# Kernel optimization log

Hardware: AMD Instinct MI355X
Metric: run time of the kernel (lower is better)

## Reference

```python
import jax, jax.numpy as jnp
import numpy as np

# dims: batch B, tokens T, model_dim D, expert hidden H, experts E, top-k K
B, T, D, H, E, K = 4, 2048, 2048, 2048, 8, 2
CAP_FACTOR = 1.0
S = B * T
C = int(np.ceil(K * S / E * CAP_FACTOR))  # per-expert capacity = 2048


def setup_inputs() -> dict:
    key = jax.random.key(0)
    k0, k1, k2, k3 = jax.random.split(key, 4)
    x = jax.random.normal(k0, (B, T, D), dtype=jnp.float32)
    wg = jax.random.normal(k1, (D, E), dtype=jnp.float32) * (D ** -0.5)
    w1 = jax.random.normal(k2, (E, D, H), dtype=jnp.float32) * (D ** -0.5)
    b1 = jnp.zeros((E, H), dtype=jnp.float32)
    w2 = jax.random.normal(k3, (E, H, D), dtype=jnp.float32) * (H ** -0.5)
    b2 = jnp.zeros((E, D), dtype=jnp.float32)
    return {"x": x, "wg": wg, "w1": w1, "b1": b1, "w2": w2, "b2": b2}


def _moe(x, wg, w1, b1, w2, b2):
    xt = x.reshape(S, D)
    # --- top-k gating (deepspeed-style, gates normalized over selected k) ---
    gates = jax.nn.softmax(xt @ wg, axis=-1)            # [S,E]
    vals, idx = jax.lax.top_k(gates, K)                 # [S,K]
    vals = vals / jnp.sum(vals, axis=-1, keepdims=True)
    # --- capacity-aware slot assignment (slot j offset by counts of slots < j) ---
    m = jax.nn.one_hot(idx, E, dtype=jnp.int32).transpose(1, 0, 2)  # [K,S,E]
    within = jnp.cumsum(m, axis=1) - m                  # 0-based rank within expert per slot
    counts = jnp.sum(m, axis=1)                         # [K,E]
    offs = jnp.cumsum(counts, axis=0) - counts          # [K,E] offsets from earlier slots
    loc = jnp.sum((within + offs[:, None, :]) * m, axis=2)  # [K,S]
    eid = idx.T                                         # [K,S]
    valid = loc < C
    loc_c = jnp.minimum(loc, C - 1)
    # --- dispatch: scatter raw tokens into [E,C,D] expert buffers ---
    contrib = jnp.where(valid[..., None], xt[None, :, :], 0.0)   # [K,S,D]
    disp = jnp.zeros((E, C, D), x.dtype).at[eid, loc_c].add(contrib)
    # --- grouped expert FFN: relu(x @ W1 + b1) @ W2 + b2 ---
    h = jax.nn.relu(jnp.einsum('ecd,edh->ech', disp, w1) + b1[:, None, :])
    ye = jnp.einsum('ech,ehd->ecd', h, w2) + b2[:, None, :]
    # --- combine: gather expert outputs, weight by normalized gates ---
    gathered = ye[eid, loc_c]                           # [K,S,D]
    w = (vals.T * valid).astype(x.dtype)                # [K,S]
    out = jnp.einsum('ks,ksd->sd', w, gathered)
    return out.reshape(B, T, D)


def reference(x, wg, w1, b1, w2, b2):
    y = _moe(x, wg, w1, b1, w2, b2)                     # [B,T,D]
    return jax.nn.log_softmax(jnp.sum(y, axis=2), axis=1)  # [B,T]
```

## Files before the change

### kernel.cpp

```cpp
#include <hip/hip_runtime.h>
#include <math.h>

#define S_TOK 8192
#define DDIM 2048
#define HDIM 2048
#define NE 8
#define CAP 2048
#define NBATCH 4
#define TT 2048

typedef _Float16 f16;
typedef _Float16 f16x4 __attribute__((ext_vector_type(4)));
typedef _Float16 f16x8 __attribute__((ext_vector_type(8)));
typedef float f32x4 __attribute__((ext_vector_type(4)));

typedef __attribute__((address_space(1))) const void* gas_ptr;
typedef __attribute__((address_space(3))) void* las_ptr;

#define W1T_BLOCKS 8192
#define W2S_BLOCKS 4096
#define GATE_BASE (W1T_BLOCKS + W2S_BLOCKS + 1)
#define K1_GRID (GATE_BASE + S_TOK / 4)

__global__ __launch_bounds__(256) void prep_kernel(const float* __restrict__ w1,
                                                   const float* __restrict__ w2,
                                                   const float* __restrict__ b2,
                                                   const float* __restrict__ x,
                                                   const float* __restrict__ wg,
                                                   int* __restrict__ eid,
                                                   float* __restrict__ wts,
                                                   int* __restrict__ slot_token,
                                                   float* __restrict__ zacc,
                                                   f16* __restrict__ W1T,
                                                   float* __restrict__ w2s,
                                                   float* __restrict__ b2s) {
  __shared__ float tile[64 * 65];
  int bid = blockIdx.x, tid = threadIdx.x;
  if (bid >= GATE_BASE) {
    int g = bid - GATE_BASE;
    if (g < 64) {
      int i = g * 256 + tid;
      slot_token[i] = 0;
      zacc[i] = 0.f;
    }
    int wid = tid >> 6;
    int lane = tid & 63;
    int s = g * 4 + wid;
    const float* xr = x + (size_t)s * DDIM;
    double acc[8];
#pragma unroll
    for (int e = 0; e < 8; ++e) acc[e] = 0.0;
    for (int d0 = 0; d0 < DDIM; d0 += 64) {
      float xs = xr[d0 + lane];
      const float4* wp = (const float4*)(wg + (size_t)(d0 + lane) * 8);
      float4 g0 = wp[0];
      float4 g1 = wp[1];
      double xd = (double)xs;
      acc[0] += xd * (double)g0.x; acc[1] += xd * (double)g0.y;
      acc[2] += xd * (double)g0.z; acc[3] += xd * (double)g0.w;
      acc[4] += xd * (double)g1.x; acc[5] += xd * (double)g1.y;
      acc[6] += xd * (double)g1.z; acc[7] += xd * (double)g1.w;
    }
#pragma unroll
    for (int e = 0; e < 8; ++e) {
      double v = acc[e];
      for (int off = 32; off > 0; off >>= 1) v += __shfl_down(v, off, 64);
      acc[e] = v;
    }
    if (lane == 0) {
      int e0 = 0; double l0 = acc[0];
      for (int e = 1; e < 8; ++e) if (acc[e] > l0) { l0 = acc[e]; e0 = e; }
      int e1 = -1; double l1 = -1e300;
      for (int e = 0; e < 8; ++e) if (e != e0 && acc[e] > l1) { l1 = acc[e]; e1 = e; }
      double pe = exp(l1 - l0);
      double inv = 1.0 / (1.0 + pe);
      eid[2 * s] = e0; eid[2 * s + 1] = e1;
      wts[2 * s] = (float)inv; wts[2 * s + 1] = (float)(pe * inv);
    }
    return;
  }
  if (bid < W1T_BLOCKS) {
    int e = bid >> 10, rem = bid & 1023;
    int d0 = (rem >> 5) << 6;
    int h0 = (rem & 31) << 6;
    const float* w1e = w1 + (size_t)e * DDIM * HDIM;
#pragma unroll
    for (int i = 0; i < 4; ++i) {
      int linear = i * 256 + tid;
      int r = linear >> 4, c4 = linear & 15;
      float4 v = *(const float4*)(w1e + (size_t)(d0 + r) * HDIM + h0 + c4 * 4);
      float* t = &tile[r * 65 + c4 * 4];
      t[0] = v.x; t[1] = v.y; t[2] = v.z; t[3] = v.w;
    }
    __syncthreads();
    f16* W1Te = W1T + (size_t)e * HDIM * DDIM;
#pragma unroll
    for (int i = 0; i < 2; ++i) {
      int linear = i * 256 + tid;
      int hr = linear >> 3, l8 = linear & 7;
      f16x8 o;
#pragma unroll
      for (int j = 0; j < 8; ++j) o[j] = (f16)tile[(l8 * 8 + j) * 65 + hr];
      *(f16x8*)(W1Te + (size_t)(h0 + hr) * DDIM + d0 + l8 * 8) = o;
    }
    return;
  }
  if (bid < W1T_BLOCKS + W2S_BLOCKS) {
    int wid = tid >> 6, lane = tid & 63;
    int row = (bid - W1T_BLOCKS) * 4 + wid;
    const float4* w24 = (const float4*)w2;
    float acc = 0.f;
    for (int j = 0; j < 8; ++j) {
      float4 v = w24[(size_t)row * 512 + j * 64 + lane];
      acc += v.x + v.y + v.z + v.w;
    }
    for (int off = 32; off > 0; off >>= 1) acc += __shfl_down(acc, off, 64);
    if (lane == 0) w2s[row] = acc;
    return;
  }
  {
    int e = tid >> 5, l32 = tid & 31;
    float acc = 0.f;
    for (int j = 0; j < 64; ++j) acc += b2[e * 2048 + j * 32 + l32];
    for (int off = 16; off > 0; off >>= 1) acc += __shfl_down(acc, off, 32);
    if (l32 == 0) b2s[e] = acc;
  }
}

__global__ __launch_bounds__(256) void scan_kernel(const int* __restrict__ eid,
                                                   int* __restrict__ locb,
                                                   int* __restrict__ slot_token) {
  __shared__ int seg[4][2][8];
  __shared__ int base[4][2][8];
  int tid = threadIdx.x, wid = tid >> 6, lane = tid & 63;
  unsigned long long lower = (lane == 0) ? 0ull : ((~0ull) >> (64 - lane));
  const int2* eid2 = (const int2*)eid;
  int c0 = 0, c1 = 0;
  for (int r = 0; r < 32; ++r) {
    int2 ee = eid2[wid * 2048 + r * 64 + lane];
#pragma unroll
    for (int e = 0; e < 8; ++e) {
      unsigned long long b0 = __ballot(ee.x == e);
      unsigned long long b1 = __ballot(ee.y == e);
      if (lane == e) { c0 += __popcll(b0); c1 += __popcll(b1); }
    }
  }
  if (lane < 8) { seg[wid][0][lane] = c0; seg[wid][1][lane] = c1; }
  __syncthreads();
  if (lane < 8) {
    int e = lane;
    int tot0 = seg[0][0][e] + seg[1][0][e] + seg[2][0][e] + seg[3][0][e];
    int b0 = 0, b1 = tot0;
    for (int w = 0; w < wid; ++w) { b0 += seg[w][0][e]; b1 += seg[w][1][e]; }
    base[wid][0][e] = b0; base[wid][1][e] = b1;
  }
  for (int r = 0; r < 32; ++r) {
    int2 ee = eid2[wid * 2048 + r * 64 + lane];
    int rank0 = 0, rank1 = 0, add0 = 0, add1 = 0;
#pragma unroll
    for (int e = 0; e < 8; ++e) {
      unsigned long long b0 = __ballot(ee.x == e);
      unsigned long long b1 = __ballot(ee.y == e);
      if (ee.x == e) rank0 = __popcll(b0 & lower);
      if (ee.y == e) rank1 = __popcll(b1 & lower);
      if (lane == e) { add0 = __popcll(b0); add1 = __popcll(b1); }
    }
    int loc0 = base[wid][0][ee.x] + rank0;
    int loc1 = base[wid][1][ee.y] + rank1;
    int s = wid * 2048 + r * 64 + lane;
    int2 lo; lo.x = loc0; lo.y = loc1;
    *(int2*)&locb[2 * s] = lo;
    if (loc0 < CAP) slot_token[ee.x * CAP + loc0] = s;
    if (loc1 < CAP) slot_token[ee.y * CAP + loc1] = s;
    if (lane < 8) {
      atomicAdd(&base[wid][0][lane], add0);
      atomicAdd(&base[wid][1][lane], add1);
    }
  }
}

__global__ __launch_bounds__(256) void abuild_kernel(const float* __restrict__ x,
                                                     const int* __restrict__ slot_token,
                                                     f16* __restrict__ A16) {
  int wid = threadIdx.x >> 6, lane = threadIdx.x & 63;
  int slot = blockIdx.x * 4 + wid;
  int s = slot_token[slot];
  const float4* x4 = (const float4*)x + (size_t)s * 512 + lane;
  f16x4* outp = (f16x4*)(A16 + (size_t)slot * DDIM) + lane;
#pragma unroll
  for (int i = 0; i < 8; ++i) {
    float4 xv = x4[i * 64];
    f16x4 h;
    h[0] = (f16)xv.x; h[1] = (f16)xv.y; h[2] = (f16)xv.z; h[3] = (f16)xv.w;
    outp[i * 64] = h;
  }
}


template <int MB, int NB>
__device__ __forceinline__ void quad_mfma(f32x4 (&acc)[8][4], const f16x8 (&av)[4][2],
                                          const f16x8 (&bv)[2][2]) {
#pragma unroll
  for (int mf = 0; mf < 4; ++mf)
#pragma unroll
    for (int nf = 0; nf < 2; ++nf) {
      f32x4 c = acc[MB + mf][NB + nf];
      c = __builtin_amdgcn_mfma_f32_16x16x32_f16(av[mf][0], bv[nf][0], c, 0, 0, 0);
      c = __builtin_amdgcn_mfma_f32_16x16x32_f16(av[mf][1], bv[nf][1], c, 0, 0, 0);
      acc[MB + mf][NB + nf] = c;
    }
}

__device__ __forceinline__ void lda4(f16x8 (&av)[4][2], const f16* p0, const f16* p1, int mh) {
#pragma unroll
  for (int mf = 0; mf < 4; ++mf) {
    av[mf][0] = *(const f16x8*)(p0 + (mh * 4 + mf) * 1024);
    av[mf][1] = *(const f16x8*)(p1 + (mh * 4 + mf) * 1024);
  }
}
__device__ __forceinline__ void ldb2(f16x8 (&bv)[2][2], const f16* p0, const f16* p1, int nh) {
#pragma unroll
  for (int nf = 0; nf < 2; ++nf) {
    bv[nf][0] = *(const f16x8*)(p0 + (nh * 2 + nf) * 1024);
    bv[nf][1] = *(const f16x8*)(p1 + (nh * 2 + nf) * 1024);
  }
}

__device__ __forceinline__ void stage_half(const f16* tile_rows, f16* lds_region,
                                           int T, int h, int wl8, int wu8, int cs) {
#pragma unroll
  for (int i = 0; i < 2; ++i) {
    const f16* g = tile_rows + (size_t)(h * 128 + i * 64 + wl8) * DDIM + T * 64 + cs * 8;
    f16* d = lds_region + (h * 128 + i * 64 + wu8) * 64;
    __builtin_amdgcn_global_load_lds((gas_ptr)g, (las_ptr)d, 16, 0, 0);
  }
}

__device__ __forceinline__ void bar() {
  asm volatile("" ::: "memory");
  __builtin_amdgcn_s_barrier();
  asm volatile("" ::: "memory");
}
__device__ __forceinline__ void mfma_open() {
  bar();
  asm volatile("s_waitcnt lgkmcnt(0)" ::: "memory");
  __builtin_amdgcn_sched_barrier(0);
  __builtin_amdgcn_s_setprio(1);
}
__device__ __forceinline__ void mfma_close() {
  __builtin_amdgcn_s_setprio(0);
  bar();
}
__device__ __forceinline__ void mfma_close_w4() {
  __builtin_amdgcn_s_setprio(0);
  asm volatile("s_waitcnt vmcnt(4)" ::: "memory");
  bar();
}
__device__ __forceinline__ void mfma_close_w0() {
  __builtin_amdgcn_s_setprio(0);
  asm volatile("s_waitcnt vmcnt(0)" ::: "memory");
  bar();
}

__global__ __launch_bounds__(512, 2) void gemm_kernel(const f16* __restrict__ A16,
                                                      const f16* __restrict__ W1T,
                                                      const float* __restrict__ b1,
                                                      const float* __restrict__ w2s,
                                                      float* __restrict__ zacc) {
  __shared__ __align__(16) f16 lds[4 * 256 * 64];
  const int tid = threadIdx.x;
  const int wid = tid >> 6, lane = tid & 63;
  const int wm = wid >> 2, wn = wid & 3;
  const int quad = lane >> 4, l15 = lane & 15;
  const int l3 = lane >> 3, c7 = lane & 7;
  const int cs = c7 ^ l3;
  const int wl8 = wid * 8 + l3, wu8 = wid * 8;

  int bid = blockIdx.x;
  int e = bid & 7;
  int idx = bid >> 3;
  int cT = idx >> 3, hT = idx & 7;
  int c0 = cT * 256, h0 = hT * 256;

  const f16* Abase = A16 + ((size_t)e * CAP + c0) * DDIM;
  const f16* Bbase = W1T + ((size_t)e * HDIM + h0) * DDIM;

  f16* bufA0 = &lds[0];
  f16* bufB0 = &lds[16384];
  f16* bufA1 = &lds[2 * 16384];
  f16* bufB1 = &lds[3 * 16384];

  const int so0 = (quad ^ c7) * 8;
  const int so1 = ((quad + 4) ^ c7) * 8;
  const f16* a0k0 = bufA0 + (wm * 128 + l15) * 64 + so0;
  const f16* a0k1 = bufA0 + (wm * 128 + l15) * 64 + so1;
  const f16* a1k0 = a0k0 + 2 * 16384;
  const f16* a1k1 = a0k1 + 2 * 16384;
  const f16* b0k0 = bufB0 + (wn * 64 + l15) * 64 + so0;
  const f16* b0k1 = bufB0 + (wn * 64 + l15) * 64 + so1;
  const f16* b1k0 = b0k0 + 2 * 16384;
  const f16* b1k1 = b0k1 + 2 * 16384;

  f32x4 acc[8][4];
#pragma unroll
  for (int i = 0; i < 8; ++i)
#pragma unroll
    for (int jj = 0; jj < 4; ++jj) acc[i][jj] = (f32x4){0.f, 0.f, 0.f, 0.f};
  f16x8 fa[4][2], fb0[2][2], fb1[2][2];

  stage_half(Abase, bufA0, 0, 0, wl8, wu8, cs);
  stage_half(Abase, bufA0, 0, 1, wl8, wu8, cs);
  stage_half(Bbase, bufB0, 0, 0, wl8, wu8, cs);
  stage_half(Bbase, bufB0, 0, 1, wl8, wu8, cs);
  stage_half(Bbase, bufB1, 1, 0, wl8, wu8, cs);
  stage_half(Bbase, bufB1, 1, 1, wl8, wu8, cs);
  asm volatile("s_waitcnt vmcnt(4)" ::: "memory");
  bar();

#pragma unroll 1
  for (int it = 0; it < 15; ++it) {
    const int Ta = 2 * it + 1, Tb = 2 * it + 2, Tc = 2 * it + 3;
    lda4(fa, a0k0, a0k1, 0);
    ldb2(fb0, b0k0, b0k1, 0);
    stage_half(Abase, bufA1, Ta, 0, wl8, wu8, cs);
    mfma_open(); quad_mfma<0, 0>(acc, fa, fb0); mfma_close();

    ldb2(fb1, b0k0, b0k1, 1);
    stage_half(Abase, bufA1, Ta, 1, wl8, wu8, cs);
    mfma_open(); quad_mfma<0, 2>(acc, fa, fb1); mfma_close();

    lda4(fa, a0k0, a0k1, 1);
    stage_half(Bbase, bufB0, Tb, 0, wl8, wu8, cs);
    mfma_open(); quad_mfma<4, 2>(acc, fa, fb1); mfma_close();

    stage_half(Bbase, bufB0, Tb, 1, wl8, wu8, cs);
    mfma_open(); quad_mfma<4, 0>(acc, fa, fb0); mfma_close_w4();

    lda4(fa, a1k0, a1k1, 0);
    ldb2(fb0, b1k0, b1k1, 0);
    stage_half(Abase, bufA0, Tb, 0, wl8, wu8, cs);
    mfma_open(); quad_mfma<0, 0>(acc, fa, fb0); mfma_close();

    ldb2(fb1, b1k0, b1k1, 1);
    stage_half(Abase, bufA0, Tb, 1, wl8, wu8, cs);
    mfma_open(); quad_mfma<0, 2>(acc, fa, fb1); mfma_close();

    lda4(fa, a1k0, a1k1, 1);
    stage_half(Bbase, bufB1, Tc, 0, wl8, wu8, cs);
    mfma_open(); quad_mfma<4, 2>(acc, fa, fb1); mfma_close();

    stage_half(Bbase, bufB1, Tc, 1, wl8, wu8, cs);
    mfma_open(); quad_mfma<4, 0>(acc, fa, fb0); mfma_close_w4();
  }
  {
    lda4(fa, a0k0, a0k1, 0);
    ldb2(fb0, b0k0, b0k1, 0);
    stage_half(Abase, bufA1, 31, 0, wl8, wu8, cs);
    mfma_open(); quad_mfma<0, 0>(acc, fa, fb0); mfma_close();

    ldb2(fb1, b0k0, b0k1, 1);
    stage_half(Abase, bufA1, 31, 1, wl8, wu8, cs);
    mfma_open(); quad_mfma<0, 2>(acc, fa, fb1); mfma_close();

    lda4(fa, a0k0, a0k1, 1);
    mfma_open(); quad_mfma<4, 2>(acc, fa, fb1); mfma_close();

    mfma_open(); quad_mfma<4, 0>(acc, fa, fb0); mfma_close_w0();

    lda4(fa, a1k0, a1k1, 0);
    ldb2(fb0, b1k0, b1k1, 0);
    mfma_open(); quad_mfma<0, 0>(acc, fa, fb0); mfma_close();

    ldb2(fb1, b1k0, b1k1, 1);
    mfma_open(); quad_mfma<0, 2>(acc, fa, fb1); mfma_close();

    lda4(fa, a1k0, a1k1, 1);
    mfma_open(); quad_mfma<4, 2>(acc, fa, fb1); mfma_close();

    mfma_open(); quad_mfma<4, 0>(acc, fa, fb0);
    __builtin_amdgcn_s_setprio(0);
  }

  float b1v[4], wsv[4];
#pragma unroll
  for (int nf = 0; nf < 4; ++nf) {
    int h = h0 + wn * 64 + nf * 16 + l15;
    b1v[nf] = b1[e * HDIM + h];
    wsv[nf] = w2s[e * HDIM + h];
  }
#pragma unroll
  for (int mf = 0; mf < 8; ++mf) {
    float pr[4];
#pragma unroll
    for (int rr = 0; rr < 4; ++rr) {
      float t = 0.f;
#pragma unroll
      for (int nf = 0; nf < 4; ++nf) {
        float v = acc[mf][nf][rr] + b1v[nf];
        t += (v > 0.f ? v : 0.f) * wsv[nf];
      }
      pr[rr] = t;
    }
#pragma unroll
    for (int rr = 0; rr < 4; ++rr)
#pragma unroll
      for (int off = 1; off < 16; off <<= 1) pr[rr] += __shfl_xor(pr[rr], off, 64);
    if (l15 == 0) {
      int m = c0 + wm * 128 + mf * 16 + quad * 4;
#pragma unroll
      for (int rr = 0; rr < 4; ++rr) atomicAdd(&zacc[e * CAP + m + rr], pr[rr]);
    }
  }
}

__global__ __launch_bounds__(1024) void tail_kernel(const int* __restrict__ eid,
                                                    const int* __restrict__ locb,
                                                    const float* __restrict__ wts,
                                                    const float* __restrict__ zacc,
                                                    const float* __restrict__ b2s,
                                                    float* __restrict__ out) {
  __shared__ float red[16];
  int b = blockIdx.x, tid = threadIdx.x;
  int wid = tid >> 6, lane = tid & 63;
  float v[2];
  float mx = -1e30f;
#pragma unroll
  for (int i = 0; i < 2; ++i) {
    int s = b * TT + i * 1024 + tid;
    float zz = 0.f;
#pragma unroll
    for (int k = 0; k < 2; ++k) {
      int e = eid[2 * s + k], loc = locb[2 * s + k];
      if (loc < CAP) zz += wts[2 * s + k] * (zacc[e * CAP + loc] + b2s[e]);
    }
    v[i] = zz;
    mx = fmaxf(mx, zz);
  }
  for (int off = 32; off > 0; off >>= 1) mx = fmaxf(mx, __shfl_xor(mx, off, 64));
  if (lane == 0) red[wid] = mx;
  __syncthreads();
  mx = red[0];
#pragma unroll
  for (int j = 1; j < 16; ++j) mx = fmaxf(mx, red[j]);
  float sum = expf(v[0] - mx) + expf(v[1] - mx);
  for (int off = 32; off > 0; off >>= 1) sum += __shfl_xor(sum, off, 64);
  __syncthreads();
  if (lane == 0) red[wid] = sum;
  __syncthreads();
  sum = 0.f;
#pragma unroll
  for (int j = 0; j < 16; ++j) sum += red[j];
  float lse = mx + logf(sum);
#pragma unroll
  for (int i = 0; i < 2; ++i) out[b * TT + i * 1024 + tid] = v[i] - lse;
}

extern "C" void kernel_launch(void* const* d_in, const int* in_sizes, int n_in,
                              void* d_out, int out_size, void* d_ws, size_t ws_size,
                              hipStream_t stream) {
  const float* x  = (const float*)d_in[0];
  const float* wg = (const float*)d_in[1];
  const float* w1 = (const float*)d_in[2];
  const float* b1 = (const float*)d_in[3];
  const float* w2 = (const float*)d_in[4];
  const float* b2 = (const float*)d_in[5];
  float* out = (float*)d_out;

  char* ws = (char*)d_ws;
  size_t off = 0;
  auto alloc = [&](size_t bytes) -> char* {
    char* p = ws + off;
    off += (bytes + 255) & ~(size_t)255;
    return p;
  };
  f16* A16 = (f16*)alloc((size_t)NE * CAP * DDIM * 2);
  f16* W1T = (f16*)alloc((size_t)NE * HDIM * DDIM * 2);
  float* w2s = (float*)alloc((size_t)NE * HDIM * 4);
  float* b2s = (float*)alloc(NE * 4);
  int* eid = (int*)alloc((size_t)S_TOK * 2 * 4);
  float* wts = (float*)alloc((size_t)S_TOK * 2 * 4);
  int* locb = (int*)alloc((size_t)S_TOK * 2 * 4);
  int* slot_token = (int*)alloc((size_t)NE * CAP * 4);
  float* zacc = (float*)alloc((size_t)NE * CAP * 4);
  if (off > ws_size) return;

  prep_kernel<<<K1_GRID, 256, 0, stream>>>(w1, w2, b2, x, wg, eid, wts, slot_token, zacc,
                                           W1T, w2s, b2s);
  scan_kernel<<<1, 256, 0, stream>>>(eid, locb, slot_token);
  abuild_kernel<<<NE * CAP / 4, 256, 0, stream>>>(x, slot_token, A16);
  gemm_kernel<<<NE * 64, 512, 0, stream>>>(A16, W1T, b1, w2s, zacc);
  tail_kernel<<<NBATCH, 1024, 0, stream>>>(eid, locb, wts, zacc, b2s, out);
}
```

Baseline: 541.4 us.

## Process two H tiles per GEMM block and widen scan to 1024 threads

The GEMM grid is halved so each block computes two 256-wide H tiles back to back, with the second tile's first B stages prefetched during the first tile's tail. This lets the next tile's loads overlap the drain and spreads the launch over 256 blocks, which on a 256-CU part matches a single wave. The single-block scan kernel now uses 16 waves instead of 4, shortening its serial ballot loop. The cost is fewer blocks in flight, less latency hiding, and a longer runtime per block.

```diff
diff --git a/kernel.cpp b/kernel.cpp
--- a/kernel.cpp
+++ b/kernel.cpp
@@ -127,17 +127,17 @@
   }
 }
 
-__global__ __launch_bounds__(256) void scan_kernel(const int* __restrict__ eid,
-                                                   int* __restrict__ locb,
-                                                   int* __restrict__ slot_token) {
-  __shared__ int seg[4][2][8];
-  __shared__ int base[4][2][8];
+__global__ __launch_bounds__(1024) void scan_kernel(const int* __restrict__ eid,
+                                                    int* __restrict__ locb,
+                                                    int* __restrict__ slot_token) {
+  __shared__ int seg[16][2][8];
+  __shared__ int base[16][2][8];
   int tid = threadIdx.x, wid = tid >> 6, lane = tid & 63;
   unsigned long long lower = (lane == 0) ? 0ull : ((~0ull) >> (64 - lane));
   const int2* eid2 = (const int2*)eid;
   int c0 = 0, c1 = 0;
-  for (int r = 0; r < 32; ++r) {
-    int2 ee = eid2[wid * 2048 + r * 64 + lane];
+  for (int r = 0; r < 8; ++r) {
+    int2 ee = eid2[wid * 512 + r * 64 + lane];
 #pragma unroll
     for (int e = 0; e < 8; ++e) {
       unsigned long long b0 = __ballot(ee.x == e);
@@ -149,13 +149,15 @@
   __syncthreads();
   if (lane < 8) {
     int e = lane;
-    int tot0 = seg[0][0][e] + seg[1][0][e] + seg[2][0][e] + seg[3][0][e];
+    int tot0 = 0;
+#pragma unroll
+    for (int w = 0; w < 16; ++w) tot0 += seg[w][0][e];
     int b0 = 0, b1 = tot0;
     for (int w = 0; w < wid; ++w) { b0 += seg[w][0][e]; b1 += seg[w][1][e]; }
     base[wid][0][e] = b0; base[wid][1][e] = b1;
   }
-  for (int r = 0; r < 32; ++r) {
-    int2 ee = eid2[wid * 2048 + r * 64 + lane];
+  for (int r = 0; r < 8; ++r) {
+    int2 ee = eid2[wid * 512 + r * 64 + lane];
     int rank0 = 0, rank1 = 0, add0 = 0, add1 = 0;
 #pragma unroll
     for (int e = 0; e < 8; ++e) {
@@ -167,7 +169,7 @@
     }
     int loc0 = base[wid][0][ee.x] + rank0;
     int loc1 = base[wid][1][ee.y] + rank1;
-    int s = wid * 2048 + r * 64 + lane;
+    int s = wid * 512 + r * 64 + lane;
     int2 lo; lo.x = loc0; lo.y = loc1;
     *(int2*)&locb[2 * s] = lo;
     if (loc0 < CAP) slot_token[ee.x * CAP + loc0] = s;
@@ -260,6 +262,88 @@
   __builtin_amdgcn_s_setprio(0);
   asm volatile("s_waitcnt vmcnt(0)" ::: "memory");
   bar();
+}
+
+struct GemmCtx {
+  const f16 *a0k0, *a0k1, *a1k0, *a1k1, *b0k0, *b0k1, *b1k0, *b1k1;
+  f16 *bufA0, *bufA1, *bufB0, *bufB1;
+  int wl8, wu8, cs;
+};
+
+__device__ __forceinline__ void loop15(const GemmCtx& c, const f16* Ab, const f16* Bb,
+                                       f32x4 (&acc)[8][4]) {
+  f16x8 fa[4][2], fb0[2][2], fb1[2][2];
+#pragma unroll 1
+  for (int it = 0; it < 15; ++it) {
+    const int Ta = 2 * it + 1, Tb = 2 * it + 2, Tc = 2 * it + 3;
+    lda4(fa, c.a0k0, c.a0k1, 0);
+    ldb2(fb0, c.b0k0, c.b0k1, 0);
+    stage_half(Ab, c.bufA1, Ta, 0, c.wl8, c.wu8, c.cs);
+    mfma_open(); quad_mfma<0, 0>(acc, fa, fb0); mfma_close();
+
+    ldb2(fb1, c.b0k0, c.b0k1, 1);
+    stage_half(Ab, c.bufA1, Ta, 1, c.wl8, c.wu8, c.cs);
+    mfma_open(); quad_mfma<0, 2>(acc, fa, fb1); mfma_close();
+
+    lda4(fa, c.a0k0, c.a0k1, 1);
+    stage_half(Bb, c.bufB0, Tb, 0, c.wl8, c.wu8, c.cs);
+    mfma_open(); quad_mfma<4, 2>(acc, fa, fb1); mfma_close();
+
+    stage_half(Bb, c.bufB0, Tb, 1, c.wl8, c.wu8, c.cs);
+    mfma_open(); quad_mfma<4, 0>(acc, fa, fb0); mfma_close_w4();
+
+    lda4(fa, c.a1k0, c.a1k1, 0);
+    ldb2(fb0, c.b1k0, c.b1k1, 0);
+    stage_half(Ab, c.bufA0, Tb, 0, c.wl8, c.wu8, c.cs);
+    mfma_open(); quad_mfma<0, 0>(acc, fa, fb0); mfma_close();
+
+    ldb2(fb1, c.b1k0, c.b1k1, 1);
+    stage_half(Ab, c.bufA0, Tb, 1, c.wl8, c.wu8, c.cs);
+    mfma_open(); quad_mfma<0, 2>(acc, fa, fb1); mfma_close();
+
+    lda4(fa, c.a1k0, c.a1k1, 1);
+    stage_half(Bb, c.bufB1, Tc, 0, c.wl8, c.wu8, c.cs);
+    mfma_open(); quad_mfma<4, 2>(acc, fa, fb1); mfma_close();
+
+    stage_half(Bb, c.bufB1, Tc, 1, c.wl8, c.wu8, c.cs);
+    mfma_open(); quad_mfma<4, 0>(acc, fa, fb0); mfma_close_w4();
+  }
+}
+
+__device__ __forceinline__ void epilogue(f32x4 (&acc)[8][4], const float* __restrict__ b1,
+                                         const float* __restrict__ w2s,
+                                         float* __restrict__ zacc, int e, int c0, int h0,
+                                         int wm, int wn, int quad, int l15) {
+  float b1v[4], wsv[4];
+#pragma unroll
+  for (int nf = 0; nf < 4; ++nf) {
+    int h = h0 + wn * 64 + nf * 16 + l15;
+    b1v[nf] = b1[e * HDIM + h];
+    wsv[nf] = w2s[e * HDIM + h];
+  }
+#pragma unroll
+  for (int mf = 0; mf < 8; ++mf) {
+    float pr[4];
+#pragma unroll
+    for (int rr = 0; rr < 4; ++rr) {
+      float t = 0.f;
+#pragma unroll
+      for (int nf = 0; nf < 4; ++nf) {
+        float v = acc[mf][nf][rr] + b1v[nf];
+        t += (v > 0.f ? v : 0.f) * wsv[nf];
+      }
+      pr[rr] = t;
+    }
+#pragma unroll
+    for (int rr = 0; rr < 4; ++rr)
+#pragma unroll
+      for (int off = 1; off < 16; off <<= 1) pr[rr] += __shfl_xor(pr[rr], off, 64);
+    if (l15 == 0) {
+      int m = c0 + wm * 128 + mf * 16 + quad * 4;
+#pragma unroll
+      for (int rr = 0; rr < 4; ++rr) atomicAdd(&zacc[e * CAP + m + rr], pr[rr]);
+    }
+  }
 }
 
 __global__ __launch_bounds__(512, 2) void gemm_kernel(const f16* __restrict__ A16,
@@ -279,138 +363,123 @@
   int bid = blockIdx.x;
   int e = bid & 7;
   int idx = bid >> 3;
-  int cT = idx >> 3, hT = idx & 7;
-  int c0 = cT * 256, h0 = hT * 256;
+  int cT = idx >> 2, hTp = idx & 3;
+  int c0 = cT * 256;
+  int h0a = hTp * 256, h0b = (hTp + 4) * 256;
 
   const f16* Abase = A16 + ((size_t)e * CAP + c0) * DDIM;
-  const f16* Bbase = W1T + ((size_t)e * HDIM + h0) * DDIM;
-
-  f16* bufA0 = &lds[0];
-  f16* bufB0 = &lds[16384];
-  f16* bufA1 = &lds[2 * 16384];
-  f16* bufB1 = &lds[3 * 16384];
+  const f16* Bbase0 = W1T + ((size_t)e * HDIM + h0a) * DDIM;
+  const f16* Bbase1 = W1T + ((size_t)e * HDIM + h0b) * DDIM;
+
+  GemmCtx c;
+  c.bufA0 = &lds[0];
+  c.bufB0 = &lds[16384];
+  c.bufA1 = &lds[2 * 16384];
+  c.bufB1 = &lds[3 * 16384];
+  c.wl8 = wl8; c.wu8 = wu8; c.cs = cs;
 
   const int so0 = (quad ^ c7) * 8;
   const int so1 = ((quad + 4) ^ c7) * 8;
-  const f16* a0k0 = bufA0 + (wm * 128 + l15) * 64 + so0;
-  const f16* a0k1 = bufA0 + (wm * 128 + l15) * 64 + so1;
-  const f16* a1k0 = a0k0 + 2 * 16384;
-  const f16* a1k1 = a0k1 + 2 * 16384;
-  const f16* b0k0 = bufB0 + (wn * 64 + l15) * 64 + so0;
-  const f16* b0k1 = bufB0 + (wn * 64 + l15) * 64 + so1;
-  const f16* b1k0 = b0k0 + 2 * 16384;
-  const f16* b1k1 = b0k1 + 2 * 16384;
+  c.a0k0 = c.bufA0 + (wm * 128 + l15) * 64 + so0;
+  c.a0k1 = c.bufA0 + (wm * 128 + l15) * 64 + so1;
+  c.a1k0 = c.a0k0 + 2 * 16384;
+  c.a1k1 = c.a0k1 + 2 * 16384;
+  c.b0k0 = c.bufB0 + (wn * 64 + l15) * 64 + so0;
+  c.b0k1 = c.bufB0 + (wn * 64 + l15) * 64 + so1;
+  c.b1k0 = c.b0k0 + 2 * 16384;
+  c.b1k1 = c.b0k1 + 2 * 16384;
 
   f32x4 acc[8][4];
 #pragma unroll
   for (int i = 0; i < 8; ++i)
 #pragma unroll
     for (int jj = 0; jj < 4; ++jj) acc[i][jj] = (f32x4){0.f, 0.f, 0.f, 0.f};
-  f16x8 fa[4][2], fb0[2][2], fb1[2][2];
-
-  stage_half(Abase, bufA0, 0, 0, wl8, wu8, cs);
-  stage_half(Abase, bufA0, 0, 1, wl8, wu8, cs);
-  stage_half(Bbase, bufB0, 0, 0, wl8, wu8, cs);
-  stage_half(Bbase, bufB0, 0, 1, wl8, wu8, cs);
-  stage_half(Bbase, bufB1, 1, 0, wl8, wu8, cs);
-  stage_half(Bbase, bufB1, 1, 1, wl8, wu8, cs);
+
+  stage_half(Abase, c.bufA0, 0, 0, wl8, wu8, cs);
+  stage_half(Abase, c.bufA0, 0, 1, wl8, wu8, cs);
+  stage_half(Bbase0, c.bufB0, 0, 0, wl8, wu8, cs);
+  stage_half(Bbase0, c.bufB0, 0, 1, wl8, wu8, cs);
+  stage_half(Bbase0, c.bufB1, 1, 0, wl8, wu8, cs);
+  stage_half(Bbase0, c.bufB1, 1, 1, wl8, wu8, cs);
   asm volatile("s_waitcnt vmcnt(4)" ::: "memory");
   bar();
 
-#pragma unroll 1
-  for (int it = 0; it < 15; ++it) {
-    const int Ta = 2 * it + 1, Tb = 2 * it + 2, Tc = 2 * it + 3;
-    lda4(fa, a0k0, a0k1, 0);
-    ldb2(fb0, b0k0, b0k1, 0);
-    stage_half(Abase, bufA1, Ta, 0, wl8, wu8, cs);
+  loop15(c, Abase, Bbase0, acc);
+
+  {
+    f16x8 fa[4][2], fb0[2][2], fb1[2][2];
+    lda4(fa, c.a0k0, c.a0k1, 0);
+    ldb2(fb0, c.b0k0, c.b0k1, 0);
+    stage_half(Abase, c.bufA1, 31, 0, wl8, wu8, cs);
     mfma_open(); quad_mfma<0, 0>(acc, fa, fb0); mfma_close();
 
-    ldb2(fb1, b0k0, b0k1, 1);
-    stage_half(Abase, bufA1, Ta, 1, wl8, wu8, cs);
+    ldb2(fb1, c.b0k0, c.b0k1, 1);
+    stage_half(Abase, c.bufA1, 31, 1, wl8, wu8, cs);
     mfma_open(); quad_mfma<0, 2>(acc, fa, fb1); mfma_close();
 
-    lda4(fa, a0k0, a0k1, 1);
-    stage_half(Bbase, bufB0, Tb, 0, wl8, wu8, cs);
+    lda4(fa, c.a0k0, c.a0k1, 1);
+    stage_half(Bbase1, c.bufB0, 0, 0, wl8, wu8, cs);
     mfma_open(); quad_mfma<4, 2>(acc, fa, fb1); mfma_close();
 
-    stage_half(Bbase, bufB0, Tb, 1, wl8, wu8, cs);
+    stage_half(Bbase1, c.bufB0, 0, 1, wl8, wu8, cs);
     mfma_open(); quad_mfma<4, 0>(acc, fa, fb0); mfma_close_w4();
 
-    lda4(fa, a1k0, a1k1, 0);
-    ldb2(fb0, b1k0, b1k1, 0);
-    stage_half(Abase, bufA0, Tb, 0, wl8, wu8, cs);
+    lda4(fa, c.a1k0, c.a1k1, 0);
+    ldb2(fb0, c.b1k0, c.b1k1, 0);
+    stage_half(Abase, c.bufA0, 0, 0, wl8, wu8, cs);
     mfma_open(); quad_mfma<0, 0>(acc, fa, fb0); mfma_close();
 
-    ldb2(fb1, b1k0, b1k1, 1);
-    stage_half(Abase, bufA0, Tb, 1, wl8, wu8, cs);
+    ldb2(fb1, c.b1k0, c.b1k1, 1);
+    stage_half(Abase, c.bufA0, 0, 1, wl8, wu8, cs);
     mfma_open(); quad_mfma<0, 2>(acc, fa, fb1); mfma_close();
 
-    lda4(fa, a1k0, a1k1, 1);
-    stage_half(Bbase, bufB1, Tc, 0, wl8, wu8, cs);
+    lda4(fa, c.a1k0, c.a1k1, 1);
+    stage_half(Bbase1, c.bufB1, 1, 0, wl8, wu8, cs);
     mfma_open(); quad_mfma<4, 2>(acc, fa, fb1); mfma_close();
 
-    stage_half(Bbase, bufB1, Tc, 1, wl8, wu8, cs);
+    stage_half(Bbase1, c.bufB1, 1, 1, wl8, wu8, cs);
     mfma_open(); quad_mfma<4, 0>(acc, fa, fb0); mfma_close_w4();
   }
+
+  epilogue(acc, b1, w2s, zacc, e, c0, h0a, wm, wn, quad, l15);
+#pragma unroll
+  for (int i = 0; i < 8; ++i)
+#pragma unroll
+    for (int jj = 0; jj < 4; ++jj) acc[i][jj] = (f32x4){0.f, 0.f, 0.f, 0.f};
+
+  loop15(c, Abase, Bbase1, acc);
+
   {
-    lda4(fa, a0k0, a0k1, 0);
-    ldb2(fb0, b0k0, b0k1, 0);
-    stage_half(Abase, bufA1, 31, 0, wl8, wu8, cs);
+    f16x8 fa[4][2], fb0[2][2], fb1[2][2];
+    lda4(fa, c.a0k0, c.a0k1, 0);
+    ldb2(fb0, c.b0k0, c.b0k1, 0);
+    stage_half(Abase, c.bufA1, 31, 0, wl8, wu8, cs);
     mfma_open(); quad_mfma<0, 0>(acc, fa, fb0); mfma_close();
 
-    ldb2(fb1, b0k0, b0k1, 1);
-    stage_half(Abase, bufA1, 31, 1, wl8, wu8, cs);
+    ldb2(fb1, c.b0k0, c.b0k1, 1);
+    stage_half(Abase, c.bufA1, 31, 1, wl8, wu8, cs);
     mfma_open(); quad_mfma<0, 2>(acc, fa, fb1); mfma_close();
 
-    lda4(fa, a0k0, a0k1, 1);
+    lda4(fa, c.a0k0, c.a0k1, 1);
     mfma_open(); quad_mfma<4, 2>(acc, fa, fb1); mfma_close();
 
     mfma_open(); quad_mfma<4, 0>(acc, fa, fb0); mfma_close_w0();
 
-    lda4(fa, a1k0, a1k1, 0);
-    ldb2(fb0, b1k0, b1k1, 0);
+    lda4(fa, c.a1k0, c.a1k1, 0);
+    ldb2(fb0, c.b1k0, c.b1k1, 0);
     mfma_open(); quad_mfma<0, 0>(acc, fa, fb0); mfma_close();
 
-    ldb2(fb1, b1k0, b1k1, 1);
+    ldb2(fb1, c.b1k0, c.b1k1, 1);
     mfma_open(); quad_mfma<0, 2>(acc, fa, fb1); mfma_close();
 
-    lda4(fa, a1k0, a1k1, 1);
+    lda4(fa, c.a1k0, c.a1k1, 1);
     mfma_open(); quad_mfma<4, 2>(acc, fa, fb1); mfma_close();
 
     mfma_open(); quad_mfma<4, 0>(acc, fa, fb0);
     __builtin_amdgcn_s_setprio(0);
   }
 
-  float b1v[4], wsv[4];
-#pragma unroll
-  for (int nf = 0; nf < 4; ++nf) {
-    int h = h0 + wn * 64 + nf * 16 + l15;
-    b1v[nf] = b1[e * HDIM + h];
-    wsv[nf] = w2s[e * HDIM + h];
-  }
-#pragma unroll
-  for (int mf = 0; mf < 8; ++mf) {
-    float pr[4];
-#pragma unroll
-    for (int rr = 0; rr < 4; ++rr) {
-      float t = 0.f;
-#pragma unroll
-      for (int nf = 0; nf < 4; ++nf) {
-        float v = acc[mf][nf][rr] + b1v[nf];
-        t += (v > 0.f ? v : 0.f) * wsv[nf];
-      }
-      pr[rr] = t;
-    }
-#pragma unroll
-    for (int rr = 0; rr < 4; ++rr)
-#pragma unroll
-      for (int off = 1; off < 16; off <<= 1) pr[rr] += __shfl_xor(pr[rr], off, 64);
-    if (l15 == 0) {
-      int m = c0 + wm * 128 + mf * 16 + quad * 4;
-#pragma unroll
-      for (int rr = 0; rr < 4; ++rr) atomicAdd(&zacc[e * CAP + m + rr], pr[rr]);
-    }
-  }
+  epilogue(acc, b1, w2s, zacc, e, c0, h0b, wm, wn, quad, l15);
 }
 
 __global__ __launch_bounds__(1024) void tail_kernel(const int* __restrict__ eid,
@@ -486,8 +555,8 @@
 
   prep_kernel<<<K1_GRID, 256, 0, stream>>>(w1, w2, b2, x, wg, eid, wts, slot_token, zacc,
                                            W1T, w2s, b2s);
-  scan_kernel<<<1, 256, 0, stream>>>(eid, locb, slot_token);
+  scan_kernel<<<1, 1024, 0, stream>>>(eid, locb, slot_token);
   abuild_kernel<<<NE * CAP / 4, 256, 0, stream>>>(x, slot_token, A16);
-  gemm_kernel<<<NE * 64, 512, 0, stream>>>(A16, W1T, b1, w2s, zacc);
+  gemm_kernel<<<NE * 32, 512, 0, stream>>>(A16, W1T, b1, w2s, zacc);
   tail_kernel<<<NBATCH, 1024, 0, stream>>>(eid, locb, wts, zacc, b2s, out);
 }
```

Measured after the change: 527.2 us. -2.6%, faster.

## Persist GEMM blocks over two H tiles, restructure k-tile pipeline, widen scan

Applied to the files above, without the earlier changes.

The GEMM grid is halved so each block computes two 256-wide H tiles in sequence. The second tile's first K slice is prefetched during the first tile's last iteration, and the prologue is only paid once per pair. The K loop is rewritten as a templated ktile step that stages a full A/B tile ahead and prefetches the next B fragment, with fewer barriers. The single-block scan now uses 16 waves instead of 4, which shortens its serial loop. The trade-off is 256 blocks (one wave on 256 CUs) instead of 512, which may hurt load balance or latency hiding.

```diff
diff --git a/kernel.cpp b/kernel.cpp
--- a/kernel.cpp
+++ b/kernel.cpp
@@ -127,17 +127,17 @@
   }
 }
 
-__global__ __launch_bounds__(256) void scan_kernel(const int* __restrict__ eid,
-                                                   int* __restrict__ locb,
-                                                   int* __restrict__ slot_token) {
-  __shared__ int seg[4][2][8];
-  __shared__ int base[4][2][8];
+__global__ __launch_bounds__(1024) void scan_kernel(const int* __restrict__ eid,
+                                                    int* __restrict__ locb,
+                                                    int* __restrict__ slot_token) {
+  __shared__ int seg[16][2][8];
+  __shared__ int base[16][2][8];
   int tid = threadIdx.x, wid = tid >> 6, lane = tid & 63;
   unsigned long long lower = (lane == 0) ? 0ull : ((~0ull) >> (64 - lane));
   const int2* eid2 = (const int2*)eid;
   int c0 = 0, c1 = 0;
-  for (int r = 0; r < 32; ++r) {
-    int2 ee = eid2[wid * 2048 + r * 64 + lane];
+  for (int r = 0; r < 8; ++r) {
+    int2 ee = eid2[wid * 512 + r * 64 + lane];
 #pragma unroll
     for (int e = 0; e < 8; ++e) {
       unsigned long long b0 = __ballot(ee.x == e);
@@ -149,13 +149,15 @@
   __syncthreads();
   if (lane < 8) {
     int e = lane;
-    int tot0 = seg[0][0][e] + seg[1][0][e] + seg[2][0][e] + seg[3][0][e];
+    int tot0 = 0;
+#pragma unroll
+    for (int w = 0; w < 16; ++w) tot0 += seg[w][0][e];
     int b0 = 0, b1 = tot0;
     for (int w = 0; w < wid; ++w) { b0 += seg[w][0][e]; b1 += seg[w][1][e]; }
     base[wid][0][e] = b0; base[wid][1][e] = b1;
   }
-  for (int r = 0; r < 32; ++r) {
-    int2 ee = eid2[wid * 2048 + r * 64 + lane];
+  for (int r = 0; r < 8; ++r) {
+    int2 ee = eid2[wid * 512 + r * 64 + lane];
     int rank0 = 0, rank1 = 0, add0 = 0, add1 = 0;
 #pragma unroll
     for (int e = 0; e < 8; ++e) {
@@ -167,7 +169,7 @@
     }
     int loc0 = base[wid][0][ee.x] + rank0;
     int loc1 = base[wid][1][ee.y] + rank1;
-    int s = wid * 2048 + r * 64 + lane;
+    int s = wid * 512 + r * 64 + lane;
     int2 lo; lo.x = loc0; lo.y = loc1;
     *(int2*)&locb[2 * s] = lo;
     if (loc0 < CAP) slot_token[ee.x * CAP + loc0] = s;
@@ -241,25 +243,85 @@
   __builtin_amdgcn_s_barrier();
   asm volatile("" ::: "memory");
 }
-__device__ __forceinline__ void mfma_open() {
-  bar();
+__device__ __forceinline__ void lgkm0sb() {
   asm volatile("s_waitcnt lgkmcnt(0)" ::: "memory");
   __builtin_amdgcn_sched_barrier(0);
+}
+
+template <bool STAGE, bool PREF>
+__device__ __forceinline__ void ktile(const f16* aRk0, const f16* aRk1,
+                                      const f16* bRk0, const f16* bRk1,
+                                      const f16* nbk0, const f16* nbk1,
+                                      f16* stA, f16* stB,
+                                      const f16* srcA, const f16* srcB, int Ta, int Tb,
+                                      int wl8, int wu8, int cs,
+                                      f16x8 (&fa)[4][2], f16x8 (&fb0)[2][2],
+                                      f16x8 (&fb1)[2][2], f32x4 (&acc)[8][4]) {
+  bar();
+  if (STAGE) {
+    stage_half(srcB, stB, Tb, 0, wl8, wu8, cs);
+    stage_half(srcB, stB, Tb, 1, wl8, wu8, cs);
+    stage_half(srcA, stA, Ta, 0, wl8, wu8, cs);
+    stage_half(srcA, stA, Ta, 1, wl8, wu8, cs);
+  }
+  lda4(fa, aRk0, aRk1, 0);
+  lgkm0sb();
   __builtin_amdgcn_s_setprio(1);
-}
-__device__ __forceinline__ void mfma_close() {
+  quad_mfma<0, 0>(acc, fa, fb0);
   __builtin_amdgcn_s_setprio(0);
+  ldb2(fb1, bRk0, bRk1, 1);
+  lgkm0sb();
+  __builtin_amdgcn_s_setprio(1);
+  quad_mfma<0, 2>(acc, fa, fb1);
+  __builtin_amdgcn_s_setprio(0);
+  lda4(fa, aRk0, aRk1, 1);
+  lgkm0sb();
+  __builtin_amdgcn_s_setprio(1);
+  quad_mfma<4, 0>(acc, fa, fb0);
+  __builtin_amdgcn_s_setprio(0);
+  if (STAGE) asm volatile("s_waitcnt vmcnt(4)" ::: "memory");
   bar();
-}
-__device__ __forceinline__ void mfma_close_w4() {
+  if (PREF) ldb2(fb0, nbk0, nbk1, 0);
+  __builtin_amdgcn_s_setprio(1);
+  quad_mfma<4, 2>(acc, fa, fb1);
   __builtin_amdgcn_s_setprio(0);
-  asm volatile("s_waitcnt vmcnt(4)" ::: "memory");
-  bar();
-}
-__device__ __forceinline__ void mfma_close_w0() {
-  __builtin_amdgcn_s_setprio(0);
-  asm volatile("s_waitcnt vmcnt(0)" ::: "memory");
-  bar();
+  if (STAGE) asm volatile("s_waitcnt vmcnt(0)" ::: "memory");
+}
+
+__device__ __forceinline__ void epilogue(f32x4 (&acc)[8][4], const float* __restrict__ b1,
+                                         const float* __restrict__ w2s,
+                                         float* __restrict__ zacc, int e, int c0, int h0,
+                                         int wm, int wn, int quad, int l15) {
+  float b1v[4], wsv[4];
+#pragma unroll
+  for (int nf = 0; nf < 4; ++nf) {
+    int h = h0 + wn * 64 + nf * 16 + l15;
+    b1v[nf] = b1[e * HDIM + h];
+    wsv[nf] = w2s[e * HDIM + h];
+  }
+#pragma unroll
+  for (int mf = 0; mf < 8; ++mf) {
+    float pr[4];
+#pragma unroll
+    for (int rr = 0; rr < 4; ++rr) {
+      float t = 0.f;
+#pragma unroll
+      for (int nf = 0; nf < 4; ++nf) {
+        float v = acc[mf][nf][rr] + b1v[nf];
+        t += (v > 0.f ? v : 0.f) * wsv[nf];
+      }
+      pr[rr] = t;
+    }
+#pragma unroll
+    for (int rr = 0; rr < 4; ++rr)
+#pragma unroll
+      for (int off = 1; off < 16; off <<= 1) pr[rr] += __shfl_xor(pr[rr], off, 64);
+    if (l15 == 0) {
+      int m = c0 + wm * 128 + mf * 16 + quad * 4;
+#pragma unroll
+      for (int rr = 0; rr < 4; ++rr) atomicAdd(&zacc[e * CAP + m + rr], pr[rr]);
+    }
+  }
 }
 
 __global__ __launch_bounds__(512, 2) void gemm_kernel(const f16* __restrict__ A16,
@@ -279,11 +341,13 @@
   int bid = blockIdx.x;
   int e = bid & 7;
   int idx = bid >> 3;
-  int cT = idx >> 3, hT = idx & 7;
-  int c0 = cT * 256, h0 = hT * 256;
+  int cT = idx >> 2, hTp = idx & 3;
+  int c0 = cT * 256;
+  int h0a = hTp * 256, h0b = (hTp + 4) * 256;
 
   const f16* Abase = A16 + ((size_t)e * CAP + c0) * DDIM;
-  const f16* Bbase = W1T + ((size_t)e * HDIM + h0) * DDIM;
+  const f16* Bbase0 = W1T + ((size_t)e * HDIM + h0a) * DDIM;
+  const f16* Bbase1 = W1T + ((size_t)e * HDIM + h0b) * DDIM;
 
   f16* bufA0 = &lds[0];
   f16* bufB0 = &lds[16384];
@@ -308,109 +372,45 @@
     for (int jj = 0; jj < 4; ++jj) acc[i][jj] = (f32x4){0.f, 0.f, 0.f, 0.f};
   f16x8 fa[4][2], fb0[2][2], fb1[2][2];
 
+  stage_half(Bbase0, bufB0, 0, 0, wl8, wu8, cs);
+  stage_half(Bbase0, bufB0, 0, 1, wl8, wu8, cs);
   stage_half(Abase, bufA0, 0, 0, wl8, wu8, cs);
   stage_half(Abase, bufA0, 0, 1, wl8, wu8, cs);
-  stage_half(Bbase, bufB0, 0, 0, wl8, wu8, cs);
-  stage_half(Bbase, bufB0, 0, 1, wl8, wu8, cs);
-  stage_half(Bbase, bufB1, 1, 0, wl8, wu8, cs);
-  stage_half(Bbase, bufB1, 1, 1, wl8, wu8, cs);
-  asm volatile("s_waitcnt vmcnt(4)" ::: "memory");
+  asm volatile("s_waitcnt vmcnt(0)" ::: "memory");
   bar();
+  ldb2(fb0, b0k0, b0k1, 0);
 
 #pragma unroll 1
   for (int it = 0; it < 15; ++it) {
-    const int Ta = 2 * it + 1, Tb = 2 * it + 2, Tc = 2 * it + 3;
-    lda4(fa, a0k0, a0k1, 0);
-    ldb2(fb0, b0k0, b0k1, 0);
-    stage_half(Abase, bufA1, Ta, 0, wl8, wu8, cs);
-    mfma_open(); quad_mfma<0, 0>(acc, fa, fb0); mfma_close();
-
-    ldb2(fb1, b0k0, b0k1, 1);
-    stage_half(Abase, bufA1, Ta, 1, wl8, wu8, cs);
-    mfma_open(); quad_mfma<0, 2>(acc, fa, fb1); mfma_close();
-
-    lda4(fa, a0k0, a0k1, 1);
-    stage_half(Bbase, bufB0, Tb, 0, wl8, wu8, cs);
-    mfma_open(); quad_mfma<4, 2>(acc, fa, fb1); mfma_close();
-
-    stage_half(Bbase, bufB0, Tb, 1, wl8, wu8, cs);
-    mfma_open(); quad_mfma<4, 0>(acc, fa, fb0); mfma_close_w4();
-
-    lda4(fa, a1k0, a1k1, 0);
-    ldb2(fb0, b1k0, b1k1, 0);
-    stage_half(Abase, bufA0, Tb, 0, wl8, wu8, cs);
-    mfma_open(); quad_mfma<0, 0>(acc, fa, fb0); mfma_close();
-
-    ldb2(fb1, b1k0, b1k1, 1);
-    stage_half(Abase, bufA0, Tb, 1, wl8, wu8, cs);
-    mfma_open(); quad_mfma<0, 2>(acc, fa, fb1); mfma_close();
-
-    lda4(fa, a1k0, a1k1, 1);
-    stage_half(Bbase, bufB1, Tc, 0, wl8, wu8, cs);
-    mfma_open(); quad_mfma<4, 2>(acc, fa, fb1); mfma_close();
-
-    stage_half(Bbase, bufB1, Tc, 1, wl8, wu8, cs);
-    mfma_open(); quad_mfma<4, 0>(acc, fa, fb0); mfma_close_w4();
-  }
-  {
-    lda4(fa, a0k0, a0k1, 0);
-    ldb2(fb0, b0k0, b0k1, 0);
-    stage_half(Abase, bufA1, 31, 0, wl8, wu8, cs);
-    mfma_open(); quad_mfma<0, 0>(acc, fa, fb0); mfma_close();
-
-    ldb2(fb1, b0k0, b0k1, 1);
-    stage_half(Abase, bufA1, 31, 1, wl8, wu8, cs);
-    mfma_open(); quad_mfma<0, 2>(acc, fa, fb1); mfma_close();
-
-    lda4(fa, a0k0, a0k1, 1);
-    mfma_open(); quad_mfma<4, 2>(acc, fa, fb1); mfma_close();
-
-    mfma_open(); quad_mfma<4, 0>(acc, fa, fb0); mfma_close_w0();
-
-    lda4(fa, a1k0, a1k1, 0);
-    ldb2(fb0, b1k0, b1k1, 0);
-    mfma_open(); quad_mfma<0, 0>(acc, fa, fb0); mfma_close();
-
-    ldb2(fb1, b1k0, b1k1, 1);
-    mfma_open(); quad_mfma<0, 2>(acc, fa, fb1); mfma_close();
-
-    lda4(fa, a1k0, a1k1, 1);
-    mfma_open(); quad_mfma<4, 2>(acc, fa, fb1); mfma_close();
-
-    mfma_open(); quad_mfma<4, 0>(acc, fa, fb0);
-    __builtin_amdgcn_s_setprio(0);
-  }
-
-  float b1v[4], wsv[4];
-#pragma unroll
-  for (int nf = 0; nf < 4; ++nf) {
-    int h = h0 + wn * 64 + nf * 16 + l15;
-    b1v[nf] = b1[e * HDIM + h];
-    wsv[nf] = w2s[e * HDIM + h];
-  }
-#pragma unroll
-  for (int mf = 0; mf < 8; ++mf) {
-    float pr[4];
-#pragma unroll
-    for (int rr = 0; rr < 4; ++rr) {
-      float t = 0.f;
-#pragma unroll
-      for (int nf = 0; nf < 4; ++nf) {
-        float v = acc[mf][nf][rr] + b1v[nf];
-        t += (v > 0.f ? v : 0.f) * wsv[nf];
-      }
-      pr[rr] = t;
-    }
-#pragma unroll
-    for (int rr = 0; rr < 4; ++rr)
-#pragma unroll
-      for (int off = 1; off < 16; off <<= 1) pr[rr] += __shfl_xor(pr[rr], off, 64);
-    if (l15 == 0) {
-      int m = c0 + wm * 128 + mf * 16 + quad * 4;
-#pragma unroll
-      for (int rr = 0; rr < 4; ++rr) atomicAdd(&zacc[e * CAP + m + rr], pr[rr]);
-    }
-  }
+    ktile<true, true>(a0k0, a0k1, b0k0, b0k1, b1k0, b1k1, bufA1, bufB1,
+                      Abase, Bbase0, 2 * it + 1, 2 * it + 1, wl8, wu8, cs, fa, fb0, fb1, acc);
+    ktile<true, true>(a1k0, a1k1, b1k0, b1k1, b0k0, b0k1, bufA0, bufB0,
+                      Abase, Bbase0, 2 * it + 2, 2 * it + 2, wl8, wu8, cs, fa, fb0, fb1, acc);
+  }
+  ktile<true, true>(a0k0, a0k1, b0k0, b0k1, b1k0, b1k1, bufA1, bufB1,
+                    Abase, Bbase0, 31, 31, wl8, wu8, cs, fa, fb0, fb1, acc);
+  ktile<true, true>(a1k0, a1k1, b1k0, b1k1, b0k0, b0k1, bufA0, bufB0,
+                    Abase, Bbase1, 0, 0, wl8, wu8, cs, fa, fb0, fb1, acc);
+
+  epilogue(acc, b1, w2s, zacc, e, c0, h0a, wm, wn, quad, l15);
+#pragma unroll
+  for (int i = 0; i < 8; ++i)
+#pragma unroll
+    for (int jj = 0; jj < 4; ++jj) acc[i][jj] = (f32x4){0.f, 0.f, 0.f, 0.f};
+
+#pragma unroll 1
+  for (int it = 0; it < 15; ++it) {
+    ktile<true, true>(a0k0, a0k1, b0k0, b0k1, b1k0, b1k1, bufA1, bufB1,
+                      Abase, Bbase1, 2 * it + 1, 2 * it + 1, wl8, wu8, cs, fa, fb0, fb1, acc);
+    ktile<true, true>(a1k0, a1k1, b1k0, b1k1, b0k0, b0k1, bufA0, bufB0,
+                      Abase, Bbase1, 2 * it + 2, 2 * it + 2, wl8, wu8, cs, fa, fb0, fb1, acc);
+  }
+  ktile<true, true>(a0k0, a0k1, b0k0, b0k1, b1k0, b1k1, bufA1, bufB1,
+                    Abase, Bbase1, 31, 31, wl8, wu8, cs, fa, fb0, fb1, acc);
+  ktile<false, false>(a1k0, a1k1, b1k0, b1k1, b0k0, b0k1, bufA0, bufB0,
+                      Abase, Bbase1, 0, 0, wl8, wu8, cs, fa, fb0, fb1, acc);
+
+  epilogue(acc, b1, w2s, zacc, e, c0, h0b, wm, wn, quad, l15);
 }
 
 __global__ __launch_bounds__(1024) void tail_kernel(const int* __restrict__ eid,
@@ -486,8 +486,8 @@
 
   prep_kernel<<<K1_GRID, 256, 0, stream>>>(w1, w2, b2, x, wg, eid, wts, slot_token, zacc,
                                            W1T, w2s, b2s);
-  scan_kernel<<<1, 256, 0, stream>>>(eid, locb, slot_token);
+  scan_kernel<<<1, 1024, 0, stream>>>(eid, locb, slot_token);
   abuild_kernel<<<NE * CAP / 4, 256, 0, stream>>>(x, slot_token, A16);
-  gemm_kernel<<<NE * 64, 512, 0, stream>>>(A16, W1T, b1, w2s, zacc);
+  gemm_kernel<<<NE * 32, 512, 0, stream>>>(A16, W1T, b1, w2s, zacc);
   tail_kernel<<<NBATCH, 1024, 0, stream>>>(eid, locb, wts, zacc, b2s, out);
 }
```

After: 571.9 us. 1.06x slower.
